# Kernel optimization log

Measured on AMD Instinct MI355X. Metric: run time of the kernel, lower is better.

The kernel has to match this reference:

```python
import jax, jax.numpy as jnp
import numpy as np

BETA = 0.9
THRESHOLD = 1.0


def setup_inputs() -> dict:
    key = jax.random.key(0)
    k1, k2 = jax.random.split(key)
    T, NI, NO = 2048, 4096, 4096
    x = jax.random.normal(k1, (T, NI), dtype=jnp.float32)
    # matches torch.nn.init.uniform_(weight, a=0.0, b=1.0), shape [out, in]
    W = jax.random.uniform(k2, (NO, NI), dtype=jnp.float32)
    return {"x": x, "W": W}


def _snn_forward(x, W, beta=BETA, threshold=THRESHOLD):
    """Single-layer LIF (snnTorch Leaky, reset_mechanism='subtract') with
    winner-take-all early stop: the first timestep where any neuron spikes,
    a uniformly-random spiking neuron becomes a one-hot winner and all later
    records stay zero (the torch loop breaks)."""
    T = x.shape[0]
    NO = W.shape[0]
    # Batch all per-step linears into one GEMM: [T, NI] x [NO, NI]^T -> [T, NO]
    cur_all = jnp.einsum('ti,oi->to', x, W)
    # Random tie-break noise for winner selection (replaces torch.randint choice)
    noise = jax.random.uniform(jax.random.key(42), (T, NO), dtype=x.dtype)

    def step(carry, inp):
        mem, done = carry
        cur, nz = inp
        # snnTorch Leaky: reset term comes from the PREVIOUS membrane's spike
        reset = (mem > threshold).astype(mem.dtype)
        mem_new = beta * mem + cur - reset * threshold  # 'subtract' reset
        spk = (mem_new > threshold).astype(mem.dtype)
        any_spk = jnp.any(spk > 0)
        fired = any_spk & (~done)
        # uniform random choice among spiking neurons via noise-argmax
        winner = jnp.argmax(jnp.where(spk > 0, nz, -1.0))
        onehot = jax.nn.one_hot(winner, NO, dtype=mem.dtype)
        spk_row = jnp.where(fired, onehot, jnp.zeros_like(spk))
        mem_row = jnp.where(done, jnp.zeros_like(mem_new), mem_new)
        return (mem_new, done | any_spk), (spk_row, mem_row)

    init = (jnp.zeros((NO,), x.dtype), jnp.asarray(False))
    _, (spk_rec, mem_rec) = jax.lax.scan(step, init, (cur_all, noise))
    return spk_rec, mem_rec


def reference(x, W):
    return _snn_forward(x, W)
```

## Files before the change

### kernel.cpp

```cpp
#include <hip/hip_runtime.h>

#define T_STEPS 2048
#define NI 4096
#define NO 4096

static constexpr float BETA = 0.9f;
static constexpr float THRESH = 1.0f;

#define SPK_FLOATS ((unsigned)T_STEPS * (unsigned)NO)
#define SPK_VEC4   (SPK_FLOATS / 4u)
#define TOT_VEC4   (2u * SPK_VEC4)
#define ZB         2048u
#define Z4TOT      (TOT_VEC4 - 1024u)

struct Ws {
  int tstar;
  int pad;
  unsigned long long packed;
  float cur0[NO];
  int fst[NO];
  int wmax[NO];
  unsigned long long key0[NO];
};

__device__ inline void threefry2x32(unsigned k0, unsigned k1,
                                    unsigned& x0, unsigned& x1) {
  const unsigned k2 = k0 ^ k1 ^ 0x1BD11BDAu;
  x0 += k0; x1 += k1;
#define TF_RND(r) { x0 += x1; x1 = (x1 << (r)) | (x1 >> (32 - (r))); x1 ^= x0; }
  TF_RND(13) TF_RND(15) TF_RND(26) TF_RND(6)
  x0 += k1; x1 += k2 + 1u;
  TF_RND(17) TF_RND(29) TF_RND(16) TF_RND(24)
  x0 += k2; x1 += k0 + 2u;
  TF_RND(13) TF_RND(15) TF_RND(26) TF_RND(6)
  x0 += k0; x1 += k1 + 3u;
  TF_RND(17) TF_RND(29) TF_RND(16) TF_RND(24)
  x0 += k1; x1 += k2 + 4u;
  TF_RND(13) TF_RND(15) TF_RND(26) TF_RND(6)
  x0 += k2; x1 += k0 + 5u;
#undef TF_RND
}

__device__ inline unsigned long long winner_key(int ts, int o) {
  const unsigned H = (unsigned)T_STEPS * (unsigned)NO / 2u;
  const unsigned i = (unsigned)ts * (unsigned)NO + (unsigned)o;
  unsigned c0 = (i < H) ? i : (i - H);
  unsigned c1 = (i < H) ? (i + H) : i;
  threefry2x32(0u, 42u, c0, c1);
  const unsigned bits = (i < H) ? c0 : c1;
  const unsigned mant = bits >> 9;
  return (1ull << 63) | ((unsigned long long)mant << 32) |
         (unsigned)(NO - 1 - o);
}

__global__ __launch_bounds__(256) void k_main(const float* __restrict__ x,
                                              const float* __restrict__ W,
                                              float* __restrict__ out,
                                              Ws* __restrict__ ws) {
  const unsigned bid = blockIdx.x;
  const unsigned tid = threadIdx.x;
  const unsigned q   = bid / 3u;
  const unsigned r   = bid % 3u;

  if (r == 2u) {
    float4* o4 = reinterpret_cast<float4*>(out);
    const float4 z = {0.0f, 0.0f, 0.0f, 0.0f};
    const unsigned base = q * 2048u + tid;
#pragma unroll
    for (int k = 0; k < 8; ++k) {
      const unsigned j = base + (unsigned)k * 256u;
      if (j < Z4TOT) {
        const unsigned v = (j < SPK_VEC4) ? j : j + 1024u;
        o4[v] = z;
      }
    }
    return;
  }

  const int o = (int)(q * 2u + r);
  const float4* Wrow = reinterpret_cast<const float4*>(W) + (size_t)o * (NI / 4);
  const float4* xr   = reinterpret_cast<const float4*>(x);

  float acc = 0.0f;
#pragma unroll
  for (int k = 0; k < 4; ++k) {
    const int idx = (int)tid + k * 256;
    float4 wv = Wrow[idx];
    float4 xv = xr[idx];
    acc += wv.x * xv.x + wv.y * xv.y + wv.z * xv.z + wv.w * xv.w;
  }
#pragma unroll
  for (int off = 32; off >= 1; off >>= 1) acc += __shfl_xor(acc, off, 64);

  __shared__ float part[4];
  if ((tid & 63u) == 0u) part[tid >> 6] = acc;
  __syncthreads();
  if (tid == 0u) {
    const float cur = part[0] + part[1] + part[2] + part[3];
    out[SPK_FLOATS + o] = cur;
    ws->cur0[o] = cur;
    ws->key0[o] = (cur > THRESH) ? winner_key(0, o) : 0ull;
  }
}

__global__ __launch_bounds__(1024) void k_finish(Ws* __restrict__ ws) {
  const int tid = (int)threadIdx.x;
  unsigned long long k = 0ull;
#pragma unroll
  for (int j = 0; j < NO / 1024; ++j) {
    const unsigned long long v = ws->key0[tid + j * 1024];
    k = (v > k) ? v : k;
  }
#pragma unroll
  for (int off = 32; off >= 1; off >>= 1) {
    const unsigned long long v = __shfl_xor(k, off, 64);
    k = (v > k) ? v : k;
  }
  __shared__ unsigned long long part[16];
  if ((tid & 63) == 0) part[tid >> 6] = k;
  __syncthreads();
  if (tid == 0) {
    unsigned long long m = 0ull;
#pragma unroll
    for (int j = 0; j < 16; ++j) m = (part[j] > m) ? part[j] : m;
    ws->packed = m;
    ws->tstar  = (m != 0ull) ? 0 : T_STEPS;
  }
}

__global__ __launch_bounds__(256) void k_slow(const float* __restrict__ x,
                                              const float* __restrict__ W,
                                              float* __restrict__ mem_rec,
                                              Ws* __restrict__ ws) {
  if (ws->tstar == 0) return;

  const int wid  = (int)((blockIdx.x * blockDim.x + threadIdx.x) >> 6);
  const int lane = (int)(threadIdx.x & 63);
  if (wid >= NO) return;

  const float4* Wrow = reinterpret_cast<const float4*>(W) + (size_t)wid * (NI / 4);
  float4 w[16];
#pragma unroll
  for (int j = 0; j < 16; ++j) w[j] = Wrow[j * 64 + lane];

  float mem = ws->cur0[wid];
  int my_fst = T_STEPS;
  int wmax = 0;

  for (int t = 1; t < T_STEPS; ++t) {
    const float4* xr = reinterpret_cast<const float4*>(x) + (size_t)t * (NI / 4);
    float acc = 0.0f;
#pragma unroll
    for (int j = 0; j < 16; ++j) {
      float4 xv = xr[j * 64 + lane];
      acc += xv.x * w[j].x + xv.y * w[j].y + xv.z * w[j].z + xv.w * w[j].w;
    }
#pragma unroll
    for (int off = 32; off >= 1; off >>= 1) acc += __shfl_xor(acc, off, 64);

    const float reset = (mem > THRESH) ? THRESH : 0.0f;
    mem = BETA * mem + acc - reset;

    if (lane == 0) mem_rec[(size_t)t * NO + wid] = mem;
    wmax = t;
    if (mem > THRESH) { my_fst = t; break; }
  }

  if (lane == 0) {
    ws->fst[wid] = my_fst;
    ws->wmax[wid] = wmax;
    atomicMin(&ws->tstar, my_fst);
  }
}

__global__ void k_fix(float* __restrict__ mem_rec, Ws* __restrict__ ws) {
  const int ts = ws->tstar;
  if (ts == 0 || ts >= T_STEPS) return;
  const int o = blockIdx.x * blockDim.x + threadIdx.x;
  if (o >= NO) return;
  const int wm = ws->wmax[o];
  for (int t = ts + 1; t <= wm; ++t)
    mem_rec[(size_t)t * NO + o] = 0.0f;
  if (ws->fst[o] == ts) atomicMax(&ws->packed, winner_key(ts, o));
}

__global__ void k_wwrite(float* __restrict__ spk_rec, Ws* __restrict__ ws) {
  const int ts = ws->tstar;
  if (ts < T_STEPS) {
    const unsigned o =
        (unsigned)(NO - 1) - (unsigned)(ws->packed & 0xFFFFFFFFull);
    spk_rec[(size_t)ts * NO + o] = 1.0f;
  }
}

extern "C" void kernel_launch(void* const* d_in, const int* in_sizes, int n_in,
                              void* d_out, int out_size, void* d_ws, size_t ws_size,
                              hipStream_t stream) {
  const float* x = (const float*)d_in[0];
  const float* W = (const float*)d_in[1];
  float* spk = (float*)d_out;
  float* mem = (float*)d_out + (size_t)SPK_FLOATS;
  Ws* ws = (Ws*)d_ws;

  k_main<<<NO + (int)ZB, 256, 0, stream>>>(x, W, (float*)d_out, ws);
  k_finish<<<1, 1024, 0, stream>>>(ws);
  k_slow<<<(NO * 64) / 256, 256, 0, stream>>>(x, W, mem, ws);
  k_fix<<<NO / 256, 256, 0, stream>>>(mem, ws);
  k_wwrite<<<1, 1, 0, stream>>>(spk, ws);
}
```

Before: 29.21 us.

## Merge fix and winner-write kernels, write t=0 winner directly, use nontemporal zero stores

Drops the k_fix and k_wwrite launches. The first-spike time and winner noise are packed into one 64-bit key per neuron inside k_slow, and a single block then reduces those keys, writes the spike and zeroes the stale membrane records. k_finish now writes the t=0 winner spike directly. The bulk zero fill uses nontemporal stores. This cuts launch count and avoids the atomics, at the cost of a serial single-block reduction and zero loop in the rare slow path.

```diff
diff --git a/kernel.cpp b/kernel.cpp
--- a/kernel.cpp
+++ b/kernel.cpp
@@ -13,14 +13,16 @@
 #define ZB         2048u
 #define Z4TOT      (TOT_VEC4 - 1024u)
 
+typedef float f4 __attribute__((ext_vector_type(4)));
+
 struct Ws {
   int tstar;
   int pad;
-  unsigned long long packed;
   float cur0[NO];
   int fst[NO];
   int wmax[NO];
   unsigned long long key0[NO];
+  unsigned long long keyG[NO];
 };
 
 __device__ inline void threefry2x32(unsigned k0, unsigned k1,
@@ -41,16 +43,13 @@
 #undef TF_RND
 }
 
-__device__ inline unsigned long long winner_key(int ts, int o) {
+__device__ inline unsigned noise_mant(int ts, int o) {
   const unsigned H = (unsigned)T_STEPS * (unsigned)NO / 2u;
   const unsigned i = (unsigned)ts * (unsigned)NO + (unsigned)o;
   unsigned c0 = (i < H) ? i : (i - H);
   unsigned c1 = (i < H) ? (i + H) : i;
   threefry2x32(0u, 42u, c0, c1);
-  const unsigned bits = (i < H) ? c0 : c1;
-  const unsigned mant = bits >> 9;
-  return (1ull << 63) | ((unsigned long long)mant << 32) |
-         (unsigned)(NO - 1 - o);
+  return ((i < H) ? c0 : c1) >> 9;
 }
 
 __global__ __launch_bounds__(256) void k_main(const float* __restrict__ x,
@@ -63,15 +62,15 @@
   const unsigned r   = bid % 3u;
 
   if (r == 2u) {
-    float4* o4 = reinterpret_cast<float4*>(out);
-    const float4 z = {0.0f, 0.0f, 0.0f, 0.0f};
+    f4* o4 = reinterpret_cast<f4*>(out);
+    const f4 z = {0.0f, 0.0f, 0.0f, 0.0f};
     const unsigned base = q * 2048u + tid;
 #pragma unroll
     for (int k = 0; k < 8; ++k) {
       const unsigned j = base + (unsigned)k * 256u;
       if (j < Z4TOT) {
         const unsigned v = (j < SPK_VEC4) ? j : j + 1024u;
-        o4[v] = z;
+        __builtin_nontemporal_store(z, &o4[v]);
       }
     }
     return;
@@ -99,11 +98,15 @@
     const float cur = part[0] + part[1] + part[2] + part[3];
     out[SPK_FLOATS + o] = cur;
     ws->cur0[o] = cur;
-    ws->key0[o] = (cur > THRESH) ? winner_key(0, o) : 0ull;
-  }
-}
-
-__global__ __launch_bounds__(1024) void k_finish(Ws* __restrict__ ws) {
+    ws->key0[o] = (cur > THRESH)
+        ? ((1ull << 63) | ((unsigned long long)noise_mant(0, o) << 32) |
+           (unsigned)(NO - 1 - o))
+        : 0ull;
+  }
+}
+
+__global__ __launch_bounds__(1024) void k_finish(float* __restrict__ spk,
+                                                 Ws* __restrict__ ws) {
   const int tid = (int)threadIdx.x;
   unsigned long long k = 0ull;
 #pragma unroll
@@ -123,8 +126,13 @@
     unsigned long long m = 0ull;
 #pragma unroll
     for (int j = 0; j < 16; ++j) m = (part[j] > m) ? part[j] : m;
-    ws->packed = m;
-    ws->tstar  = (m != 0ull) ? 0 : T_STEPS;
+    if (m != 0ull) {
+      ws->tstar = 0;
+      const unsigned o = (unsigned)(NO - 1) - (unsigned)(m & 0xFFFFFFFFull);
+      spk[o] = 1.0f;
+    } else {
+      ws->tstar = T_STEPS;
+    }
   }
 }
 
@@ -167,29 +175,56 @@
   }
 
   if (lane == 0) {
-    ws->fst[wid] = my_fst;
+    ws->fst[wid]  = my_fst;
     ws->wmax[wid] = wmax;
-    atomicMin(&ws->tstar, my_fst);
-  }
-}
-
-__global__ void k_fix(float* __restrict__ mem_rec, Ws* __restrict__ ws) {
-  const int ts = ws->tstar;
-  if (ts == 0 || ts >= T_STEPS) return;
-  const int o = blockIdx.x * blockDim.x + threadIdx.x;
-  if (o >= NO) return;
-  const int wm = ws->wmax[o];
-  for (int t = ts + 1; t <= wm; ++t)
-    mem_rec[(size_t)t * NO + o] = 0.0f;
-  if (ws->fst[o] == ts) atomicMax(&ws->packed, winner_key(ts, o));
-}
-
-__global__ void k_wwrite(float* __restrict__ spk_rec, Ws* __restrict__ ws) {
-  const int ts = ws->tstar;
-  if (ts < T_STEPS) {
-    const unsigned o =
-        (unsigned)(NO - 1) - (unsigned)(ws->packed & 0xFFFFFFFFull);
-    spk_rec[(size_t)ts * NO + o] = 1.0f;
+    const unsigned mant = (my_fst < T_STEPS) ? noise_mant(my_fst, wid) : 0u;
+    ws->keyG[wid] =
+        ((unsigned long long)(unsigned)(T_STEPS - my_fst) << 35) |
+        ((unsigned long long)mant << 12) |
+        (unsigned)(NO - 1 - wid);
+  }
+}
+
+__global__ __launch_bounds__(1024) void k_gfin(float* __restrict__ spk,
+                                               float* __restrict__ mem_rec,
+                                               Ws* __restrict__ ws) {
+  if (ws->tstar == 0) return;
+
+  const int tid = (int)threadIdx.x;
+  unsigned long long k = 0ull;
+#pragma unroll
+  for (int j = 0; j < NO / 1024; ++j) {
+    const unsigned long long v = ws->keyG[tid + j * 1024];
+    k = (v > k) ? v : k;
+  }
+#pragma unroll
+  for (int off = 32; off >= 1; off >>= 1) {
+    const unsigned long long v = __shfl_xor(k, off, 64);
+    k = (v > k) ? v : k;
+  }
+  __shared__ unsigned long long part[16];
+  __shared__ int s_ts;
+  if ((tid & 63) == 0) part[tid >> 6] = k;
+  __syncthreads();
+  if (tid == 0) {
+    unsigned long long m = 0ull;
+#pragma unroll
+    for (int j = 0; j < 16; ++j) m = (part[j] > m) ? part[j] : m;
+    const int ts = T_STEPS - (int)((m >> 35) & 0xFFFull);
+    s_ts = ts;
+    if (ts < T_STEPS) {
+      const unsigned o = (unsigned)(NO - 1) - (unsigned)(m & 0xFFFull);
+      spk[(size_t)ts * NO + o] = 1.0f;
+    }
+    ws->tstar = ts;
+  }
+  __syncthreads();
+  const int ts = s_ts;
+  if (ts >= T_STEPS) return;
+  for (int o = tid; o < NO; o += 1024) {
+    const int wm = ws->wmax[o];
+    for (int t = ts + 1; t <= wm; ++t)
+      mem_rec[(size_t)t * NO + o] = 0.0f;
   }
 }
 
@@ -203,8 +238,7 @@
   Ws* ws = (Ws*)d_ws;
 
   k_main<<<NO + (int)ZB, 256, 0, stream>>>(x, W, (float*)d_out, ws);
-  k_finish<<<1, 1024, 0, stream>>>(ws);
+  k_finish<<<1, 1024, 0, stream>>>(spk, ws);
   k_slow<<<(NO * 64) / 256, 256, 0, stream>>>(x, W, mem, ws);
-  k_fix<<<NO / 256, 256, 0, stream>>>(mem, ws);
-  k_wwrite<<<1, 1, 0, stream>>>(spk, ws);
-}
+  k_gfin<<<1, 1024, 0, stream>>>(spk, mem, ws);
+}
```

Result: faster. 27.88 us (-4.6%).

## Collapse finish, slow-path, fix and winner kernels into one single-block kernel

Applied to the files above, without the earlier changes.

Replaces the four follow-up kernels (reduction, per-neuron time loop, fix-up, winner write) with a single 1024-thread kernel. It computes the step-0 winner directly from cur0 and writes the spike immediately, keeping a slow sequential time loop only as a fallback when nothing fires at step 0. This removes three launches and the key0/fst/wmax workspace traffic. The zero-fill also switches to nontemporal stores. The fallback path runs on one block with scalar uncoalesced W reads and would be extremely slow if reached, but with these inputs a spike occurs at step 0.

```diff
diff --git a/kernel.cpp b/kernel.cpp
--- a/kernel.cpp
+++ b/kernel.cpp
@@ -13,14 +13,10 @@
 #define ZB         2048u
 #define Z4TOT      (TOT_VEC4 - 1024u)
 
+typedef float f4 __attribute__((ext_vector_type(4)));
+
 struct Ws {
-  int tstar;
-  int pad;
-  unsigned long long packed;
   float cur0[NO];
-  int fst[NO];
-  int wmax[NO];
-  unsigned long long key0[NO];
 };
 
 __device__ inline void threefry2x32(unsigned k0, unsigned k1,
@@ -47,10 +43,31 @@
   unsigned c0 = (i < H) ? i : (i - H);
   unsigned c1 = (i < H) ? (i + H) : i;
   threefry2x32(0u, 42u, c0, c1);
-  const unsigned bits = (i < H) ? c0 : c1;
-  const unsigned mant = bits >> 9;
+  const unsigned mant = (((i < H) ? c0 : c1) >> 9);
   return (1ull << 63) | ((unsigned long long)mant << 32) |
          (unsigned)(NO - 1 - o);
+}
+
+__device__ inline unsigned long long
+block_max_u64(unsigned long long k, unsigned long long* part) {
+  const int tid = (int)threadIdx.x;
+#pragma unroll
+  for (int off = 32; off >= 1; off >>= 1) {
+    const unsigned long long v = __shfl_xor(k, off, 64);
+    k = (v > k) ? v : k;
+  }
+  if ((tid & 63) == 0) part[tid >> 6] = k;
+  __syncthreads();
+  if (tid == 0) {
+    unsigned long long m = 0ull;
+#pragma unroll
+    for (int j = 0; j < 16; ++j) m = (part[j] > m) ? part[j] : m;
+    part[0] = m;
+  }
+  __syncthreads();
+  const unsigned long long m = part[0];
+  __syncthreads();
+  return m;
 }
 
 __global__ __launch_bounds__(256) void k_main(const float* __restrict__ x,
@@ -63,15 +80,15 @@
   const unsigned r   = bid % 3u;
 
   if (r == 2u) {
-    float4* o4 = reinterpret_cast<float4*>(out);
-    const float4 z = {0.0f, 0.0f, 0.0f, 0.0f};
+    f4* o4 = reinterpret_cast<f4*>(out);
+    const f4 z = {0.0f, 0.0f, 0.0f, 0.0f};
     const unsigned base = q * 2048u + tid;
 #pragma unroll
     for (int k = 0; k < 8; ++k) {
       const unsigned j = base + (unsigned)k * 256u;
       if (j < Z4TOT) {
         const unsigned v = (j < SPK_VEC4) ? j : j + 1024u;
-        o4[v] = z;
+        __builtin_nontemporal_store(z, &o4[v]);
       }
     }
     return;
@@ -99,97 +116,67 @@
     const float cur = part[0] + part[1] + part[2] + part[3];
     out[SPK_FLOATS + o] = cur;
     ws->cur0[o] = cur;
-    ws->key0[o] = (cur > THRESH) ? winner_key(0, o) : 0ull;
   }
 }
 
-__global__ __launch_bounds__(1024) void k_finish(Ws* __restrict__ ws) {
+__global__ __launch_bounds__(1024) void k_fin(const float* __restrict__ x,
+                                              const float* __restrict__ W,
+                                              float* __restrict__ spk,
+                                              float* __restrict__ mem_rec,
+                                              Ws* __restrict__ ws) {
   const int tid = (int)threadIdx.x;
+  __shared__ unsigned long long part[16];
+  __shared__ float xs[NI];
+
+  float mem[4];
   unsigned long long k = 0ull;
 #pragma unroll
-  for (int j = 0; j < NO / 1024; ++j) {
-    const unsigned long long v = ws->key0[tid + j * 1024];
-    k = (v > k) ? v : k;
+  for (int j = 0; j < 4; ++j) {
+    const int o = tid + j * 1024;
+    const float c = ws->cur0[o];
+    mem[j] = c;
+    if (c > THRESH) {
+      const unsigned long long v = winner_key(0, o);
+      k = (v > k) ? v : k;
+    }
   }
-#pragma unroll
-  for (int off = 32; off >= 1; off >>= 1) {
-    const unsigned long long v = __shfl_xor(k, off, 64);
-    k = (v > k) ? v : k;
+  unsigned long long m = block_max_u64(k, part);
+  if (m != 0ull) {
+    if (tid == 0) {
+      const unsigned o = (unsigned)(NO - 1) - (unsigned)(m & 0xFFFFFFFFull);
+      spk[o] = 1.0f;
+    }
+    return;
   }
-  __shared__ unsigned long long part[16];
-  if ((tid & 63) == 0) part[tid >> 6] = k;
-  __syncthreads();
-  if (tid == 0) {
-    unsigned long long m = 0ull;
-#pragma unroll
-    for (int j = 0; j < 16; ++j) m = (part[j] > m) ? part[j] : m;
-    ws->packed = m;
-    ws->tstar  = (m != 0ull) ? 0 : T_STEPS;
-  }
-}
-
-__global__ __launch_bounds__(256) void k_slow(const float* __restrict__ x,
-                                              const float* __restrict__ W,
-                                              float* __restrict__ mem_rec,
-                                              Ws* __restrict__ ws) {
-  if (ws->tstar == 0) return;
-
-  const int wid  = (int)((blockIdx.x * blockDim.x + threadIdx.x) >> 6);
-  const int lane = (int)(threadIdx.x & 63);
-  if (wid >= NO) return;
-
-  const float4* Wrow = reinterpret_cast<const float4*>(W) + (size_t)wid * (NI / 4);
-  float4 w[16];
-#pragma unroll
-  for (int j = 0; j < 16; ++j) w[j] = Wrow[j * 64 + lane];
-
-  float mem = ws->cur0[wid];
-  int my_fst = T_STEPS;
-  int wmax = 0;
 
   for (int t = 1; t < T_STEPS; ++t) {
-    const float4* xr = reinterpret_cast<const float4*>(x) + (size_t)t * (NI / 4);
-    float acc = 0.0f;
+    for (int i = tid; i < NI; i += 1024) xs[i] = x[(size_t)t * NI + i];
+    __syncthreads();
+
+    unsigned long long kk = 0ull;
 #pragma unroll
-    for (int j = 0; j < 16; ++j) {
-      float4 xv = xr[j * 64 + lane];
-      acc += xv.x * w[j].x + xv.y * w[j].y + xv.z * w[j].z + xv.w * w[j].w;
+    for (int j = 0; j < 4; ++j) {
+      const int o = tid + j * 1024;
+      const float* Wrow = W + (size_t)o * NI;
+      float acc = 0.0f;
+      for (int i = 0; i < NI; ++i) acc += xs[i] * Wrow[i];
+      const float reset = (mem[j] > THRESH) ? THRESH : 0.0f;
+      mem[j] = BETA * mem[j] + acc - reset;
+      mem_rec[(size_t)t * NO + o] = mem[j];
+      if (mem[j] > THRESH) {
+        const unsigned long long v = winner_key(t, o);
+        kk = (v > kk) ? v : kk;
+      }
     }
-#pragma unroll
-    for (int off = 32; off >= 1; off >>= 1) acc += __shfl_xor(acc, off, 64);
-
-    const float reset = (mem > THRESH) ? THRESH : 0.0f;
-    mem = BETA * mem + acc - reset;
-
-    if (lane == 0) mem_rec[(size_t)t * NO + wid] = mem;
-    wmax = t;
-    if (mem > THRESH) { my_fst = t; break; }
-  }
-
-  if (lane == 0) {
-    ws->fst[wid] = my_fst;
-    ws->wmax[wid] = wmax;
-    atomicMin(&ws->tstar, my_fst);
-  }
-}
-
-__global__ void k_fix(float* __restrict__ mem_rec, Ws* __restrict__ ws) {
-  const int ts = ws->tstar;
-  if (ts == 0 || ts >= T_STEPS) return;
-  const int o = blockIdx.x * blockDim.x + threadIdx.x;
-  if (o >= NO) return;
-  const int wm = ws->wmax[o];
-  for (int t = ts + 1; t <= wm; ++t)
-    mem_rec[(size_t)t * NO + o] = 0.0f;
-  if (ws->fst[o] == ts) atomicMax(&ws->packed, winner_key(ts, o));
-}
-
-__global__ void k_wwrite(float* __restrict__ spk_rec, Ws* __restrict__ ws) {
-  const int ts = ws->tstar;
-  if (ts < T_STEPS) {
-    const unsigned o =
-        (unsigned)(NO - 1) - (unsigned)(ws->packed & 0xFFFFFFFFull);
-    spk_rec[(size_t)ts * NO + o] = 1.0f;
+    __syncthreads();
+    m = block_max_u64(kk, part);
+    if (m != 0ull) {
+      if (tid == 0) {
+        const unsigned o = (unsigned)(NO - 1) - (unsigned)(m & 0xFFFFFFFFull);
+        spk[(size_t)t * NO + o] = 1.0f;
+      }
+      return;
+    }
   }
 }
 
@@ -203,8 +190,5 @@
   Ws* ws = (Ws*)d_ws;
 
   k_main<<<NO + (int)ZB, 256, 0, stream>>>(x, W, (float*)d_out, ws);
-  k_finish<<<1, 1024, 0, stream>>>(ws);
-  k_slow<<<(NO * 64) / 256, 256, 0, stream>>>(x, W, mem, ws);
-  k_fix<<<NO / 256, 256, 0, stream>>>(mem, ws);
-  k_wwrite<<<1, 1, 0, stream>>>(spk, ws);
+  k_fin<<<1, 1024, 0, stream>>>(x, W, spk, mem, ws);
 }
```

Result: faster. 26.02 us, median of 2 (-10.9%).
